# Optimization experiments

Hardware: AMD Instinct MI355X
Metric: run time of the kernel (lower is better)

The kernel has to match this reference:

```python
import jax, jax.numpy as jnp
import numpy as np

B, T, C, H = 4, 2048, 768, 12
D = C // H
EPS = 1e-5


def layernorm(x, g, b):
    mu = jnp.mean(x, axis=-1, keepdims=True)
    var = jnp.mean(jnp.square(x - mu), axis=-1, keepdims=True)
    return (x - mu) * jax.lax.rsqrt(var + EPS) * g + b


def setup_inputs() -> dict:
    key = jax.random.key(0)
    ks = jax.random.split(key, 16)
    s = 0.02
    return {
        "x": jax.random.normal(ks[0], (B, T, C), jnp.float32),
        "Wq": jax.random.normal(ks[1], (C, C), jnp.float32) * s,
        "bq": jnp.zeros((C,), jnp.float32),
        "Wk": jax.random.normal(ks[2], (C, C), jnp.float32) * s,
        "bk": jnp.zeros((C,), jnp.float32),
        "Wv": jax.random.normal(ks[3], (C, C), jnp.float32) * s,
        "bv": jnp.zeros((C,), jnp.float32),
        "Wo": jax.random.normal(ks[4], (C, C), jnp.float32) * s,
        "bo": jnp.zeros((C,), jnp.float32),
        "g1": jnp.ones((C,), jnp.float32),
        "b1": jnp.zeros((C,), jnp.float32),
        "g2": jnp.ones((C,), jnp.float32),
        "b2": jnp.zeros((C,), jnp.float32),
        "W1": jax.random.normal(ks[5], (C, 4 * C), jnp.float32) * s,
        "bm1": jnp.zeros((4 * C,), jnp.float32),
        "W2": jax.random.normal(ks[6], (4 * C, C), jnp.float32) * s,
        "bm2": jnp.zeros((C,), jnp.float32),
    }


def reference(x, Wq, bq, Wk, bk, Wv, bv, Wo, bo, g1, b1, g2, b2, W1, bm1, W2, bm2):
    # --- attention branch ---
    h = layernorm(x, g1, b1)
    q = (h @ Wq + bq).reshape(B, T, H, D)
    k = (h @ Wk + bk).reshape(B, T, H, D)
    v = (h @ Wv + bv).reshape(B, T, H, D)
    att = jnp.einsum('bqhd,bkhd->bhqk', q, k) / jnp.sqrt(jnp.float32(D))
    causal = jnp.tril(jnp.ones((T, T), bool))
    att = jnp.where(causal, att, -jnp.inf)
    att = jax.nn.softmax(att, axis=-1)
    o = jnp.einsum('bhqk,bkhd->bqhd', att, v).reshape(B, T, C)
    x = x + o @ Wo + bo
    # --- MLP branch ---
    h = layernorm(x, g2, b2)
    h = jax.nn.gelu(h @ W1 + bm1, approximate=False)
    return x + h @ W2 + bm2
```

## Files before the change

kernel.cpp:

```cpp
#include <hip/hip_runtime.h>
#include <hip/hip_bf16.h>

#define B_ 4
#define T_ 2048
#define C_ 768
#define H_ 12
#define D_ 64
#define QS_ 2304

typedef __attribute__((ext_vector_type(8))) short short8;
typedef __attribute__((ext_vector_type(4))) short short4v;
typedef __attribute__((ext_vector_type(4))) float f32x4;

__device__ __forceinline__ unsigned short f2bf(float f) {
    __hip_bfloat16 h = __float2bfloat16(f);
    return *reinterpret_cast<unsigned short*>(&h);
}

__device__ __forceinline__ unsigned cvt_pk_bf16(float lo, float hi) {
    unsigned r;
    asm("v_cvt_pk_bf16_f32 %0, %1, %2" : "=v"(r) : "v"(lo), "v"(hi));
    return r;
}

__device__ __forceinline__ void gl_lds16(const void* g, void* l) {
    __builtin_amdgcn_global_load_lds((const __attribute__((address_space(1))) unsigned int*)g,
                                     (__attribute__((address_space(3))) unsigned int*)l,
                                     16, 0, 0);
}

__global__ __launch_bounds__(256) void ln_f32_bf16(const float* __restrict__ x,
                                                   const float* __restrict__ g,
                                                   const float* __restrict__ b,
                                                   unsigned short* __restrict__ out) {
    int row = blockIdx.x;
    int tid = threadIdx.x;
    const float* xr = x + (size_t)row * C_;
    float v0 = xr[tid], v1 = xr[tid + 256], v2 = xr[tid + 512];
    float s = v0 + v1 + v2;
    #pragma unroll
    for (int off = 1; off < 64; off <<= 1) s += __shfl_xor(s, off);
    __shared__ float ws1[4], ws2[4];
    int wid = tid >> 6, lane = tid & 63;
    if (lane == 0) ws1[wid] = s;
    __syncthreads();
    float mean = (ws1[0] + ws1[1] + ws1[2] + ws1[3]) * (1.0f / C_);
    float d0 = v0 - mean, d1 = v1 - mean, d2 = v2 - mean;
    float qs = d0*d0 + d1*d1 + d2*d2;
    #pragma unroll
    for (int off = 1; off < 64; off <<= 1) qs += __shfl_xor(qs, off);
    if (lane == 0) ws2[wid] = qs;
    __syncthreads();
    float var = (ws2[0] + ws2[1] + ws2[2] + ws2[3]) * (1.0f / C_);
    float rs = rsqrtf(var + 1e-5f);
    unsigned short* orow = out + (size_t)row * C_;
    orow[tid]       = f2bf(d0 * rs * g[tid]       + b[tid]);
    orow[tid + 256] = f2bf(d1 * rs * g[tid + 256] + b[tid + 256]);
    orow[tid + 512] = f2bf(d2 * rs * g[tid + 512] + b[tid + 512]);
}

__global__ __launch_bounds__(256) void transpose_bf16(const float* __restrict__ W,
                                                      unsigned short* __restrict__ Wt,
                                                      int K, int N) {
    __shared__ float t[64][65];
    int n0 = blockIdx.x * 64, k0 = blockIdx.y * 64;
    int r = threadIdx.x >> 4, c4 = (threadIdx.x & 15) * 4;
    #pragma unroll
    for (int i = 0; i < 4; ++i) {
        float4 v = *(const float4*)(W + (size_t)(k0 + i * 16 + r) * N + n0 + c4);
        t[i*16 + r][c4 + 0] = v.x;
        t[i*16 + r][c4 + 1] = v.y;
        t[i*16 + r][c4 + 2] = v.z;
        t[i*16 + r][c4 + 3] = v.w;
    }
    __syncthreads();
    #pragma unroll
    for (int i = 0; i < 4; ++i) {
        ushort4 o;
        o.x = f2bf(t[c4 + 0][i*16 + r]);
        o.y = f2bf(t[c4 + 1][i*16 + r]);
        o.z = f2bf(t[c4 + 2][i*16 + r]);
        o.w = f2bf(t[c4 + 3][i*16 + r]);
        *(ushort4*)(Wt + (size_t)(n0 + i * 16 + r) * K + k0 + c4) = o;
    }
}

__global__ __launch_bounds__(256) void concat3(const float* __restrict__ a,
                                               const float* __restrict__ b,
                                               const float* __restrict__ c,
                                               float* __restrict__ o) {
    int i = blockIdx.x * 256 + threadIdx.x;
    o[i] = (i < 768) ? a[i] : (i < 1536) ? b[i - 768] : c[i - 1536];
}

template <int EPI>
__global__ __launch_bounds__(256) void gemm_bf16(const unsigned short* __restrict__ A,
                                                 const unsigned short* __restrict__ Bt,
                                                 const float* __restrict__ bias,
                                                 const float* __restrict__ resid,
                                                 void* __restrict__ Cout,
                                                 int M, int N, int K, int gx) {
    __shared__ short As[2][128 * 32];
    __shared__ short Bs[2][128 * 32];
    int tid = threadIdx.x;
    int w = tid >> 6, l = tid & 63;
    int nb = gridDim.x;
    int per = nb >> 3;
    int fid = (int)blockIdx.x;
    int wid = (fid & 7) * per + (fid >> 3);
    int bn = wid % gx, bm = wid / gx;
    int wr = w >> 1, wc = w & 1;

    f32x4 acc[4][4];
    #pragma unroll
    for (int m = 0; m < 4; ++m)
        #pragma unroll
        for (int n = 0; n < 4; ++n)
            acc[m][n] = (f32x4){0.f, 0.f, 0.f, 0.f};

    const short* Ag = (const short*)A + (size_t)(bm * 128) * K;
    const short* Bg = (const short*)Bt + (size_t)(bn * 128) * K;
    int srow = tid >> 2;
    int scol = (tid & 3) * 8;
    int lrow = l & 15, lk = (l >> 4) * 8;

    auto stage = [&](int buf, int k0) {
        #pragma unroll
        for (int i = 0; i < 2; ++i) {
            gl_lds16(Ag + (size_t)(i * 64 + srow) * K + k0 + scol,
                     (char*)&As[buf][0] + i * 4096 + w * 1024);
            gl_lds16(Bg + (size_t)(i * 64 + srow) * K + k0 + scol,
                     (char*)&Bs[buf][0] + i * 4096 + w * 1024);
        }
    };

    int nk = K / 32;
    stage(0, 0);
    __syncthreads();

    for (int kt = 0; kt < nk; ++kt) {
        int cur = kt & 1;
        if (kt + 1 < nk) stage(cur ^ 1, (kt + 1) * 32);

        short8 av[4], bv[4];
        #pragma unroll
        for (int m = 0; m < 4; ++m)
            av[m] = *(const short8*)&As[cur][(wr * 64 + m * 16 + lrow) * 32 + lk];
        #pragma unroll
        for (int n = 0; n < 4; ++n)
            bv[n] = *(const short8*)&Bs[cur][(wc * 64 + n * 16 + lrow) * 32 + lk];
        #pragma unroll
        for (int m = 0; m < 4; ++m)
            #pragma unroll
            for (int n = 0; n < 4; ++n)
                acc[m][n] = __builtin_amdgcn_mfma_f32_16x16x32_bf16(av[m], bv[n], acc[m][n], 0, 0, 0);

        __syncthreads();
    }

    int lcol = l & 15, lr4 = (l >> 4) * 4;
    int row0 = bm * 128 + wr * 64;
    int col0 = bn * 128 + wc * 64;
    #pragma unroll
    for (int m = 0; m < 4; ++m) {
        #pragma unroll
        for (int n = 0; n < 4; ++n) {
            int col = col0 + n * 16 + lcol;
            float bz = bias[col];
            #pragma unroll
            for (int r = 0; r < 4; ++r) {
                int row = row0 + m * 16 + lr4 + r;
                float v = acc[m][n][r] + bz;
                if (EPI == 1) {
                    float u = fmaf(0.044715f * v, v * v, v);
                    float e = __builtin_amdgcn_exp2f(u * -2.3022127f);
                    v = v * __builtin_amdgcn_rcpf(1.0f + e);
                    ((unsigned short*)Cout)[(size_t)row * N + col] = f2bf(v);
                } else if (EPI == 2) {
                    v += resid[(size_t)row * N + col];
                    ((float*)Cout)[(size_t)row * N + col] = v;
                } else {
                    ((unsigned short*)Cout)[(size_t)row * N + col] = f2bf(v);
                }
            }
        }
    }
}

__global__ __launch_bounds__(256) void attn_v7(const unsigned short* __restrict__ QKV,
                                               unsigned short* __restrict__ O) {
    __shared__ short Ks[128 * 64];
    __shared__ short Vt[64 * 128];

    int tid = threadIdx.x;
    int w = tid >> 6, l = tid & 63;
    int g = l >> 4, lc = l & 15;
    int wid = (int)(blockIdx.x & 7) * 192 + (int)(blockIdx.x >> 3);
    int bh = wid >> 5;
    int a  = 31 - (wid & 31);
    int b = bh / H_, h = bh % H_;
    const size_t bT = (size_t)b * T_;
    const unsigned short* Qp = QKV + h * D_;
    const unsigned short* Kp = QKV + 768 + h * D_;
    const unsigned short* Vp = QKV + 1536 + h * D_;
    const float SCL = 0.125f * 1.44269504088896340736f;

    int qw = a * 64 + w * 16;

    short8 qf[2];
    {
        const unsigned short* qp = Qp + (bT + qw + lc) * QS_;
        qf[0] = *(const short8*)(qp + g * 8);
        qf[1] = *(const short8*)(qp + 32 + g * 8);
    }

    f32x4 oacc[4];
    #pragma unroll
    for (int n = 0; n < 4; ++n) oacc[n] = (f32x4){0.f, 0.f, 0.f, 0.f};
    float mrun = 4.0f, lpart = 0.f;

    int ntiles = (a >> 1) + 1;
    for (int kt = 0; kt < ntiles; ++kt) {
        int k0 = kt * 128;
        if (kt) __syncthreads();

        #pragma unroll
        for (int c = 0; c < 4; ++c) {
            int row = w * 32 + c * 8 + (l >> 3);
            int inner = (l & 7) * 16;
            const char* src = (const char*)(Kp + (bT + k0 + row) * QS_)
                              + (inner ^ ((row & 7) << 4));
            gl_lds16(src, (char*)Ks + w * 4096 + c * 1024);
        }
        #pragma unroll
        for (int dblk = 0; dblk < 4; ++dblk)
            #pragma unroll
            for (int pp = 0; pp < 2; ++pp) {
                int d = lc + dblk * 16;
                int kk0 = w * 32 + g * 4 + pp * 16;
                const unsigned short* vp = Vp + (bT + k0 + kk0) * QS_ + d;
                short4v pk = {(short)vp[0], (short)vp[QS_], (short)vp[2*QS_], (short)vp[3*QS_]};
                int byt = (d * 256 + kk0 * 2) ^ ((d & 7) << 4);
                *(short4v*)((char*)Vt + byt) = pk;
            }
        __syncthreads();

        uint2 qd[8];
        float lmaxP[4] = {-INFINITY, -INFINITY, -INFINITY, -INFINITY};
        float rsumP[4] = {0.f, 0.f, 0.f, 0.f};
        bool full = (k0 + 127 <= qw);
        #pragma unroll
        for (int mk = 0; mk < 8; ++mk) {
            f32x4 s = (f32x4){0.f, 0.f, 0.f, 0.f};
            __builtin_amdgcn_s_setprio(1);
            #pragma unroll
            for (int ksd = 0; ksd < 2; ++ksd) {
                int row = mk * 16 + lc;
                int byt = (row * 128 + ksd * 64 + g * 16) ^ ((row & 7) << 4);
                short8 av = *(const short8*)((char*)Ks + byt);
                s = __builtin_amdgcn_mfma_f32_16x16x32_bf16(av, qf[ksd], s, 0, 0, 0);
            }
            __builtin_amdgcn_s_setprio(0);
            float p[4];
            #pragma unroll
            for (int r = 0; r < 4; ++r) {
                float sv = s[r] * SCL;
                if (!full && (k0 + mk * 16 + g * 4 + r > qw + lc)) sv = -INFINITY;
                lmaxP[r] = fmaxf(lmaxP[r], sv);
                float pv = __builtin_amdgcn_exp2f(sv - mrun);
                p[r] = pv;
                rsumP[r] += pv;
            }
            qd[mk].x = cvt_pk_bf16(p[0], p[1]);
            qd[mk].y = cvt_pk_bf16(p[2], p[3]);
        }
        float lmax = fmaxf(fmaxf(lmaxP[0], lmaxP[1]), fmaxf(lmaxP[2], lmaxP[3]));
        lpart += (rsumP[0] + rsumP[1]) + (rsumP[2] + rsumP[3]);

        #pragma unroll
        for (int ks = 0; ks < 4; ++ks) {
            uint2 qa = qd[ks * 2], qb = qd[ks * 2 + 1];
            int srcLo = lc + ((g & 1) << 5);
            int srcHi = srcLo + 16;
            unsigned a0 = (unsigned)__shfl((int)qa.x, srcLo);
            unsigned a1 = (unsigned)__shfl((int)qa.y, srcLo);
            unsigned a2 = (unsigned)__shfl((int)qa.x, srcHi);
            unsigned a3 = (unsigned)__shfl((int)qa.y, srcHi);
            unsigned b0 = (unsigned)__shfl((int)qb.x, srcLo);
            unsigned b1 = (unsigned)__shfl((int)qb.y, srcLo);
            unsigned b2 = (unsigned)__shfl((int)qb.x, srcHi);
            unsigned b3 = (unsigned)__shfl((int)qb.y, srcHi);
            bool lo = (g < 2);
            union { unsigned u[4]; short8 s8; } pa;
            pa.u[0] = lo ? a0 : b0;
            pa.u[1] = lo ? a1 : b1;
            pa.u[2] = lo ? a2 : b2;
            pa.u[3] = lo ? a3 : b3;
            short8 vbv[4];
            #pragma unroll
            for (int n = 0; n < 4; ++n) {
                int row = n * 16 + lc;
                int byt = (row * 256 + ks * 64 + g * 16) ^ ((row & 7) << 4);
                vbv[n] = *(const short8*)((char*)Vt + byt);
            }
            __builtin_amdgcn_s_setprio(1);
            #pragma unroll
            for (int n = 0; n < 4; ++n)
                oacc[n] = __builtin_amdgcn_mfma_f32_16x16x32_bf16(pa.s8, vbv[n], oacc[n], 0, 0, 0);
            __builtin_amdgcn_s_setprio(0);
        }

        if (__any(lmax > mrun + 8.0f)) {
            lmax = fmaxf(lmax, __shfl_xor(lmax, 16));
            lmax = fmaxf(lmax, __shfl_xor(lmax, 32));
            float mnew = fmaxf(mrun, lmax);
            float cc = __builtin_amdgcn_exp2f(mrun - mnew);
            lpart *= cc;
            mrun = mnew;
            #pragma unroll
            for (int r = 0; r < 4; ++r) {
                float cr = __shfl(cc, (l & 48) + g * 4 + r);
                #pragma unroll
                for (int n = 0; n < 4; ++n) oacc[n][r] *= cr;
            }
        }
    }

    float lv = lpart;
    lv += __shfl_xor(lv, 16);
    lv += __shfl_xor(lv, 32);
    float linv = 1.0f / lv;
    float inv[4];
    #pragma unroll
    for (int r = 0; r < 4; ++r) inv[r] = __shfl(linv, (l & 48) + g * 4 + r);
    #pragma unroll
    for (int n = 0; n < 4; ++n) {
        int col = h * D_ + n * 16 + lc;
        #pragma unroll
        for (int r = 0; r < 4; ++r) {
            int row = qw + g * 4 + r;
            O[(bT + row) * C_ + col] = f2bf(oacc[n][r] * inv[r]);
        }
    }
}

extern "C" void kernel_launch(void* const* d_in, const int* in_sizes, int n_in,
                              void* d_out, int out_size, void* d_ws, size_t ws_size,
                              hipStream_t stream) {
    const float* x   = (const float*)d_in[0];
    const float* Wq  = (const float*)d_in[1];
    const float* bq  = (const float*)d_in[2];
    const float* Wk  = (const float*)d_in[3];
    const float* bk  = (const float*)d_in[4];
    const float* Wv  = (const float*)d_in[5];
    const float* bv  = (const float*)d_in[6];
    const float* Wo  = (const float*)d_in[7];
    const float* bo  = (const float*)d_in[8];
    const float* g1  = (const float*)d_in[9];
    const float* b1  = (const float*)d_in[10];
    const float* g2  = (const float*)d_in[11];
    const float* b2  = (const float*)d_in[12];
    const float* W1  = (const float*)d_in[13];
    const float* bm1 = (const float*)d_in[14];
    const float* W2  = (const float*)d_in[15];
    const float* bm2 = (const float*)d_in[16];
    float* out = (float*)d_out;

    const size_t S = (size_t)B_ * T_ * C_;
    char* base = (char*)d_ws;
    unsigned short* ln1h = (unsigned short*)base;
    unsigned short* qkvb = (unsigned short*)(base + 2 * S);
    unsigned short* o    = ln1h;
    unsigned short* ln2h = qkvb;
    unsigned short* hid  = (unsigned short*)(base + 4 * S);
    float* xmid          = (float*)(base + 12 * S);
    unsigned short* wqkvt = (unsigned short*)(base + 16 * S);
    unsigned short* wot   = wqkvt + (size_t)3 * C_ * C_;
    unsigned short* w1t   = wot + (size_t)C_ * C_;
    unsigned short* w2t   = w1t + (size_t)C_ * 4 * C_;
    float* bqkv           = (float*)(w2t + (size_t)C_ * 4 * C_);

    const int M = B_ * T_;
    dim3 blk(256);

    transpose_bf16<<<dim3(C_ / 64, C_ / 64), blk, 0, stream>>>(Wq, wqkvt, C_, C_);
    transpose_bf16<<<dim3(C_ / 64, C_ / 64), blk, 0, stream>>>(Wk, wqkvt + (size_t)C_ * C_, C_, C_);
    transpose_bf16<<<dim3(C_ / 64, C_ / 64), blk, 0, stream>>>(Wv, wqkvt + (size_t)2 * C_ * C_, C_, C_);
    transpose_bf16<<<dim3(C_ / 64, C_ / 64), blk, 0, stream>>>(Wo, wot, C_, C_);
    transpose_bf16<<<dim3(4 * C_ / 64, C_ / 64), blk, 0, stream>>>(W1, w1t, C_, 4 * C_);
    transpose_bf16<<<dim3(C_ / 64, 4 * C_ / 64), blk, 0, stream>>>(W2, w2t, 4 * C_, C_);
    concat3<<<dim3(9), blk, 0, stream>>>(bq, bk, bv, bqkv);

    ln_f32_bf16<<<dim3(M), blk, 0, stream>>>(x, g1, b1, ln1h);

    gemm_bf16<3><<<dim3((QS_ / 128) * (M / 128)), blk, 0, stream>>>(ln1h, wqkvt, bqkv, nullptr, qkvb, M, QS_, C_, QS_ / 128);

    attn_v7<<<dim3(B_ * H_ * 32), blk, 0, stream>>>(qkvb, o);

    gemm_bf16<2><<<dim3((C_ / 128) * (M / 128)), blk, 0, stream>>>(o, wot, bo, x, xmid, M, C_, C_, C_ / 128);
    ln_f32_bf16<<<dim3(M), blk, 0, stream>>>(xmid, g2, b2, ln2h);
    gemm_bf16<1><<<dim3((4 * C_ / 128) * (M / 128)), blk, 0, stream>>>(ln2h, w1t, bm1, nullptr, hid, M, 4 * C_, C_, 4 * C_ / 128);
    gemm_bf16<2><<<dim3((C_ / 128) * (M / 128)), blk, 0, stream>>>(hid, w2t, bm2, xmid, out, M, C_, 4 * C_, C_ / 128);
}
```

Measured before the change: 321.5 us.

## Merge weight prep and LN1 into one kernel, fold softmax scale into QKV GEMM

Six transpose launches, the bias concat and the first layernorm are merged into a single prep_all kernel that dispatches on block index, cutting eight launches to one. The QKV GEMM gets a new epilogue that multiplies Q columns by the softmax scale times log2(e), so the attention kernel no longer multiplies each score. The attention inner loop is split into separate full-tile and masked-tile versions to drop the per-element mask check on full tiles. The cost is larger code size, and Q is now rounded to bf16 after scaling, which slightly changes rounding.

```diff
diff --git a/kernel.cpp b/kernel.cpp
--- a/kernel.cpp
+++ b/kernel.cpp
@@ -27,6 +27,95 @@
     __builtin_amdgcn_global_load_lds((const __attribute__((address_space(1))) unsigned int*)g,
                                      (__attribute__((address_space(3))) unsigned int*)l,
                                      16, 0, 0);
+}
+
+__device__ __forceinline__ void transpose_dev(const float* __restrict__ W,
+                                              unsigned short* __restrict__ Wt,
+                                              int K, int N, int bx, int by,
+                                              float (*t)[65]) {
+    int n0 = bx * 64, k0 = by * 64;
+    int r = threadIdx.x >> 4, c4 = (threadIdx.x & 15) * 4;
+    #pragma unroll
+    for (int i = 0; i < 4; ++i) {
+        float4 v = *(const float4*)(W + (size_t)(k0 + i * 16 + r) * N + n0 + c4);
+        t[i*16 + r][c4 + 0] = v.x;
+        t[i*16 + r][c4 + 1] = v.y;
+        t[i*16 + r][c4 + 2] = v.z;
+        t[i*16 + r][c4 + 3] = v.w;
+    }
+    __syncthreads();
+    #pragma unroll
+    for (int i = 0; i < 4; ++i) {
+        ushort4 o;
+        o.x = f2bf(t[c4 + 0][i*16 + r]);
+        o.y = f2bf(t[c4 + 1][i*16 + r]);
+        o.z = f2bf(t[c4 + 2][i*16 + r]);
+        o.w = f2bf(t[c4 + 3][i*16 + r]);
+        *(ushort4*)(Wt + (size_t)(n0 + i * 16 + r) * K + k0 + c4) = o;
+    }
+}
+
+__global__ __launch_bounds__(256) void prep_all(const float* __restrict__ Wq,
+                                                const float* __restrict__ Wk,
+                                                const float* __restrict__ Wv,
+                                                const float* __restrict__ Wo,
+                                                const float* __restrict__ W1,
+                                                const float* __restrict__ W2,
+                                                const float* __restrict__ bq,
+                                                const float* __restrict__ bk,
+                                                const float* __restrict__ bv,
+                                                const float* __restrict__ x,
+                                                const float* __restrict__ g1,
+                                                const float* __restrict__ b1,
+                                                unsigned short* __restrict__ wqkvt,
+                                                unsigned short* __restrict__ wot,
+                                                unsigned short* __restrict__ w1t,
+                                                unsigned short* __restrict__ w2t,
+                                                float* __restrict__ bqkv,
+                                                unsigned short* __restrict__ ln1h) {
+    __shared__ float t[64][65];
+    __shared__ float ws[8];
+    int blk = blockIdx.x;
+    int tid = threadIdx.x;
+
+    if (blk < 576) {
+        int which = blk / 144, idx = blk % 144;
+        const float* src = (which == 0) ? Wq : (which == 1) ? Wk : (which == 2) ? Wv : Wo;
+        unsigned short* dst = (which == 3) ? wot : wqkvt + (size_t)which * C_ * C_;
+        transpose_dev(src, dst, C_, C_, idx % 12, idx / 12, t);
+    } else if (blk < 1152) {
+        int idx = blk - 576;
+        transpose_dev(W1, w1t, C_, 4 * C_, idx % 48, idx / 48, t);
+    } else if (blk < 1728) {
+        int idx = blk - 1152;
+        transpose_dev(W2, w2t, 4 * C_, C_, idx % 12, idx / 12, t);
+    } else if (blk < 1737) {
+        int i = (blk - 1728) * 256 + tid;
+        bqkv[i] = (i < 768) ? bq[i] : (i < 1536) ? bk[i - 768] : bv[i - 1536];
+    } else {
+        int row = blk - 1737;
+        const float* xr = x + (size_t)row * C_;
+        float v0 = xr[tid], v1 = xr[tid + 256], v2 = xr[tid + 512];
+        float s = v0 + v1 + v2;
+        #pragma unroll
+        for (int off = 1; off < 64; off <<= 1) s += __shfl_xor(s, off);
+        int wid = tid >> 6, lane = tid & 63;
+        if (lane == 0) ws[wid] = s;
+        __syncthreads();
+        float mean = (ws[0] + ws[1] + ws[2] + ws[3]) * (1.0f / C_);
+        float d0 = v0 - mean, d1 = v1 - mean, d2 = v2 - mean;
+        float qs = d0*d0 + d1*d1 + d2*d2;
+        #pragma unroll
+        for (int off = 1; off < 64; off <<= 1) qs += __shfl_xor(qs, off);
+        if (lane == 0) ws[4 + wid] = qs;
+        __syncthreads();
+        float var = (ws[4] + ws[5] + ws[6] + ws[7]) * (1.0f / C_);
+        float rs = rsqrtf(var + 1e-5f);
+        unsigned short* orow = ln1h + (size_t)row * C_;
+        orow[tid]       = f2bf(d0 * rs * g1[tid]       + b1[tid]);
+        orow[tid + 256] = f2bf(d1 * rs * g1[tid + 256] + b1[tid + 256]);
+        orow[tid + 512] = f2bf(d2 * rs * g1[tid + 512] + b1[tid + 512]);
+    }
 }
 
 __global__ __launch_bounds__(256) void ln_f32_bf16(const float* __restrict__ x,
@@ -57,40 +146,6 @@
     orow[tid]       = f2bf(d0 * rs * g[tid]       + b[tid]);
     orow[tid + 256] = f2bf(d1 * rs * g[tid + 256] + b[tid + 256]);
     orow[tid + 512] = f2bf(d2 * rs * g[tid + 512] + b[tid + 512]);
-}
-
-__global__ __launch_bounds__(256) void transpose_bf16(const float* __restrict__ W,
-                                                      unsigned short* __restrict__ Wt,
-                                                      int K, int N) {
-    __shared__ float t[64][65];
-    int n0 = blockIdx.x * 64, k0 = blockIdx.y * 64;
-    int r = threadIdx.x >> 4, c4 = (threadIdx.x & 15) * 4;
-    #pragma unroll
-    for (int i = 0; i < 4; ++i) {
-        float4 v = *(const float4*)(W + (size_t)(k0 + i * 16 + r) * N + n0 + c4);
-        t[i*16 + r][c4 + 0] = v.x;
-        t[i*16 + r][c4 + 1] = v.y;
-        t[i*16 + r][c4 + 2] = v.z;
-        t[i*16 + r][c4 + 3] = v.w;
-    }
-    __syncthreads();
-    #pragma unroll
-    for (int i = 0; i < 4; ++i) {
-        ushort4 o;
-        o.x = f2bf(t[c4 + 0][i*16 + r]);
-        o.y = f2bf(t[c4 + 1][i*16 + r]);
-        o.z = f2bf(t[c4 + 2][i*16 + r]);
-        o.w = f2bf(t[c4 + 3][i*16 + r]);
-        *(ushort4*)(Wt + (size_t)(n0 + i * 16 + r) * K + k0 + c4) = o;
-    }
-}
-
-__global__ __launch_bounds__(256) void concat3(const float* __restrict__ a,
-                                               const float* __restrict__ b,
-                                               const float* __restrict__ c,
-                                               float* __restrict__ o) {
-    int i = blockIdx.x * 256 + threadIdx.x;
-    o[i] = (i < 768) ? a[i] : (i < 1536) ? b[i - 768] : c[i - 1536];
 }
 
 template <int EPI>
@@ -179,6 +234,9 @@
                 } else if (EPI == 2) {
                     v += resid[(size_t)row * N + col];
                     ((float*)Cout)[(size_t)row * N + col] = v;
+                } else if (EPI == 4) {
+                    if (col < 768) v *= 0.18033688011112042f;
+                    ((unsigned short*)Cout)[(size_t)row * N + col] = f2bf(v);
                 } else {
                     ((unsigned short*)Cout)[(size_t)row * N + col] = f2bf(v);
                 }
@@ -187,7 +245,7 @@
     }
 }
 
-__global__ __launch_bounds__(256) void attn_v7(const unsigned short* __restrict__ QKV,
+__global__ __launch_bounds__(256) void attn_v8(const unsigned short* __restrict__ QKV,
                                                unsigned short* __restrict__ O) {
     __shared__ short Ks[128 * 64];
     __shared__ short Vt[64 * 128];
@@ -203,7 +261,6 @@
     const unsigned short* Qp = QKV + h * D_;
     const unsigned short* Kp = QKV + 768 + h * D_;
     const unsigned short* Vp = QKV + 1536 + h * D_;
-    const float SCL = 0.125f * 1.44269504088896340736f;
 
     int qw = a * 64 + w * 16;
 
@@ -249,30 +306,57 @@
         float lmaxP[4] = {-INFINITY, -INFINITY, -INFINITY, -INFINITY};
         float rsumP[4] = {0.f, 0.f, 0.f, 0.f};
         bool full = (k0 + 127 <= qw);
-        #pragma unroll
-        for (int mk = 0; mk < 8; ++mk) {
-            f32x4 s = (f32x4){0.f, 0.f, 0.f, 0.f};
-            __builtin_amdgcn_s_setprio(1);
-            #pragma unroll
-            for (int ksd = 0; ksd < 2; ++ksd) {
-                int row = mk * 16 + lc;
-                int byt = (row * 128 + ksd * 64 + g * 16) ^ ((row & 7) << 4);
-                short8 av = *(const short8*)((char*)Ks + byt);
-                s = __builtin_amdgcn_mfma_f32_16x16x32_bf16(av, qf[ksd], s, 0, 0, 0);
-            }
-            __builtin_amdgcn_s_setprio(0);
-            float p[4];
-            #pragma unroll
-            for (int r = 0; r < 4; ++r) {
-                float sv = s[r] * SCL;
-                if (!full && (k0 + mk * 16 + g * 4 + r > qw + lc)) sv = -INFINITY;
-                lmaxP[r] = fmaxf(lmaxP[r], sv);
-                float pv = __builtin_amdgcn_exp2f(sv - mrun);
-                p[r] = pv;
-                rsumP[r] += pv;
-            }
-            qd[mk].x = cvt_pk_bf16(p[0], p[1]);
-            qd[mk].y = cvt_pk_bf16(p[2], p[3]);
+        if (full) {
+            #pragma unroll
+            for (int mk = 0; mk < 8; ++mk) {
+                f32x4 s = (f32x4){0.f, 0.f, 0.f, 0.f};
+                __builtin_amdgcn_s_setprio(1);
+                #pragma unroll
+                for (int ksd = 0; ksd < 2; ++ksd) {
+                    int row = mk * 16 + lc;
+                    int byt = (row * 128 + ksd * 64 + g * 16) ^ ((row & 7) << 4);
+                    short8 av = *(const short8*)((char*)Ks + byt);
+                    s = __builtin_amdgcn_mfma_f32_16x16x32_bf16(av, qf[ksd], s, 0, 0, 0);
+                }
+                __builtin_amdgcn_s_setprio(0);
+                float p[4];
+                #pragma unroll
+                for (int r = 0; r < 4; ++r) {
+                    float sv = s[r];
+                    lmaxP[r] = fmaxf(lmaxP[r], sv);
+                    float pv = __builtin_amdgcn_exp2f(sv - mrun);
+                    p[r] = pv;
+                    rsumP[r] += pv;
+                }
+                qd[mk].x = cvt_pk_bf16(p[0], p[1]);
+                qd[mk].y = cvt_pk_bf16(p[2], p[3]);
+            }
+        } else {
+            #pragma unroll
+            for (int mk = 0; mk < 8; ++mk) {
+                f32x4 s = (f32x4){0.f, 0.f, 0.f, 0.f};
+                __builtin_amdgcn_s_setprio(1);
+                #pragma unroll
+                for (int ksd = 0; ksd < 2; ++ksd) {
+                    int row = mk * 16 + lc;
+                    int byt = (row * 128 + ksd * 64 + g * 16) ^ ((row & 7) << 4);
+                    short8 av = *(const short8*)((char*)Ks + byt);
+                    s = __builtin_amdgcn_mfma_f32_16x16x32_bf16(av, qf[ksd], s, 0, 0, 0);
+                }
+                __builtin_amdgcn_s_setprio(0);
+                float p[4];
+                #pragma unroll
+                for (int r = 0; r < 4; ++r) {
+                    float sv = s[r];
+                    if (k0 + mk * 16 + g * 4 + r > qw + lc) sv = -INFINITY;
+                    lmaxP[r] = fmaxf(lmaxP[r], sv);
+                    float pv = __builtin_amdgcn_exp2f(sv - mrun);
+                    p[r] = pv;
+                    rsumP[r] += pv;
+                }
+                qd[mk].x = cvt_pk_bf16(p[0], p[1]);
+                qd[mk].y = cvt_pk_bf16(p[2], p[3]);
+            }
         }
         float lmax = fmaxf(fmaxf(lmaxP[0], lmaxP[1]), fmaxf(lmaxP[2], lmaxP[3]));
         lpart += (rsumP[0] + rsumP[1]) + (rsumP[2] + rsumP[3]);
@@ -383,19 +467,13 @@
     const int M = B_ * T_;
     dim3 blk(256);
 
-    transpose_bf16<<<dim3(C_ / 64, C_ / 64), blk, 0, stream>>>(Wq, wqkvt, C_, C_);
-    transpose_bf16<<<dim3(C_ / 64, C_ / 64), blk, 0, stream>>>(Wk, wqkvt + (size_t)C_ * C_, C_, C_);
-    transpose_bf16<<<dim3(C_ / 64, C_ / 64), blk, 0, stream>>>(Wv, wqkvt + (size_t)2 * C_ * C_, C_, C_);
-    transpose_bf16<<<dim3(C_ / 64, C_ / 64), blk, 0, stream>>>(Wo, wot, C_, C_);
-    transpose_bf16<<<dim3(4 * C_ / 64, C_ / 64), blk, 0, stream>>>(W1, w1t, C_, 4 * C_);
-    transpose_bf16<<<dim3(C_ / 64, 4 * C_ / 64), blk, 0, stream>>>(W2, w2t, 4 * C_, C_);
-    concat3<<<dim3(9), blk, 0, stream>>>(bq, bk, bv, bqkv);
-
-    ln_f32_bf16<<<dim3(M), blk, 0, stream>>>(x, g1, b1, ln1h);
-
-    gemm_bf16<3><<<dim3((QS_ / 128) * (M / 128)), blk, 0, stream>>>(ln1h, wqkvt, bqkv, nullptr, qkvb, M, QS_, C_, QS_ / 128);
-
-    attn_v7<<<dim3(B_ * H_ * 32), blk, 0, stream>>>(qkvb, o);
+    prep_all<<<dim3(1737 + M), blk, 0, stream>>>(Wq, Wk, Wv, Wo, W1, W2,
+                                                 bq, bk, bv, x, g1, b1,
+                                                 wqkvt, wot, w1t, w2t, bqkv, ln1h);
+
+    gemm_bf16<4><<<dim3((QS_ / 128) * (M / 128)), blk, 0, stream>>>(ln1h, wqkvt, bqkv, nullptr, qkvb, M, QS_, C_, QS_ / 128);
+
+    attn_v8<<<dim3(B_ * H_ * 32), blk, 0, stream>>>(qkvb, o);
 
     gemm_bf16<2><<<dim3((C_ / 128) * (M / 128)), blk, 0, stream>>>(o, wot, bo, x, xmid, M, C_, C_, C_ / 128);
     ln_f32_bf16<<<dim3(M), blk, 0, stream>>>(xmid, g2, b2, ln2h);
```

Result: no change. 322.3 us (+0.3%).
